# Kernel tuning notes

Measured on AMD Instinct MI355X. Metric: run time of the kernel, lower is better.

Reference implementation:

```python
import jax, jax.numpy as jnp
import numpy as np

B, S, D = 4, 1024, 1024
E, F, TOPK = 16, 512, 4


def setup_inputs() -> dict:
    key = jax.random.key(0)
    k1, k2, k3, k4, k5 = jax.random.split(key, 5)
    scale = 0.02
    return {
        "x": jax.random.normal(k1, (B, S, D), dtype=jnp.float32),
        "Wr": jax.random.normal(k2, (D, E), dtype=jnp.float32) * scale,   # router
        "Wg": jax.random.normal(k3, (E, D, F), dtype=jnp.float32) * scale,  # gate proj
        "Wu": jax.random.normal(k4, (E, D, F), dtype=jnp.float32) * scale,  # up proj
        "Wd": jax.random.normal(k5, (E, F, D), dtype=jnp.float32) * scale,  # down proj
    }


def reference(x, Wr, Wg, Wu, Wd):
    b, s, d = x.shape
    xf = x.reshape(-1, d)                      # [N, D], N = B*S
    n = xf.shape[0]
    e = Wr.shape[1]

    # --- router: softmax over experts, top-k, renormalized weights ---
    probs = jax.nn.softmax(xf @ Wr, axis=-1)   # [N, E]
    w, idx = jax.lax.top_k(probs, TOPK)        # [N, K], [N, K]
    w = w / jnp.sum(w, axis=-1, keepdims=True)

    # combine weights per (token, expert); zero for unselected experts.
    # Equivalent to the per-expert where/gather/scatter-add loop in torch.
    cw = jnp.zeros((n, e), dtype=xf.dtype).at[jnp.arange(n)[:, None], idx].add(w)

    # --- per-expert gated FFN (SwiGLU), combined with routing weights ---
    def body(acc, ws):
        wg, wu, wd, c = ws                     # [D,F], [D,F], [F,D], [N]
        h = jax.nn.silu(xf @ wg) * (xf @ wu)   # [N, F]
        return acc + c[:, None] * (h @ wd), None

    out, _ = jax.lax.scan(body, jnp.zeros_like(xf), (Wg, Wu, Wd, cw.T))
    return out.reshape(b, s, d)
```

## Files before the change

kernel.cpp:

```cpp
#include <hip/hip_runtime.h>

#define N_TOK 4096
#define DIM   1024
#define NE    16
#define NF    512
#define TOPK  4
#define CAP   4096
#define NPAIR (N_TOK * TOPK)
#define MAXTILES 144

typedef _Float16 v8h __attribute__((ext_vector_type(8)));
typedef float    v4f __attribute__((ext_vector_type(4)));

__global__ __launch_bounds__(64) void router_kernel(
    const float* __restrict__ x, const float* __restrict__ Wr,
    int* __restrict__ tokIdx, float* __restrict__ tokW)
{
    int t = blockIdx.x;
    int l = threadIdx.x;
    double z[NE];
#pragma unroll
    for (int e = 0; e < NE; e++) z[e] = 0.0;
    const float* xrow = x + (size_t)t * DIM;
#pragma unroll
    for (int i = 0; i < 16; i++) {
        int d = i * 64 + l;
        double xv = (double)xrow[d];
        const float4* wr = (const float4*)(Wr + d * NE);
        float4 w0 = wr[0], w1 = wr[1], w2 = wr[2], w3 = wr[3];
        z[0]  += xv * w0.x; z[1]  += xv * w0.y; z[2]  += xv * w0.z; z[3]  += xv * w0.w;
        z[4]  += xv * w1.x; z[5]  += xv * w1.y; z[6]  += xv * w1.z; z[7]  += xv * w1.w;
        z[8]  += xv * w2.x; z[9]  += xv * w2.y; z[10] += xv * w2.z; z[11] += xv * w2.w;
        z[12] += xv * w3.x; z[13] += xv * w3.y; z[14] += xv * w3.z; z[15] += xv * w3.w;
    }
#pragma unroll
    for (int e = 0; e < NE; e++) {
#pragma unroll
        for (int m = 1; m < 64; m <<= 1) z[e] += __shfl_xor(z[e], m, 64);
    }
    if (l == 0) {
        bool taken[NE];
#pragma unroll
        for (int e = 0; e < NE; e++) taken[e] = false;
        int idx[TOPK]; double sel[TOPK];
        for (int k = 0; k < TOPK; k++) {
            int bi = 0; double bv = -1.0e300;
            for (int e = 0; e < NE; e++)
                if (!taken[e] && z[e] > bv) { bv = z[e]; bi = e; }
            taken[bi] = true; idx[k] = bi; sel[k] = bv;
        }
        double m = sel[0];
        double ex[TOPK]; double s = 0.0;
        for (int k = 0; k < TOPK; k++) { ex[k] = exp(sel[k] - m); s += ex[k]; }
        for (int k = 0; k < TOPK; k++) {
            tokIdx[t * TOPK + k] = idx[k];
            tokW[t * TOPK + k]   = (float)(ex[k] / s);
        }
    }
}

__global__ __launch_bounds__(1024) void bin_kernel(
    const int* __restrict__ tokIdx,
    int* __restrict__ cnt, int* __restrict__ ptile,
    int* __restrict__ tileE, int* __restrict__ tileMt,
    int* __restrict__ bpair)
{
    int wv = threadIdx.x >> 6;
    int lane = threadIdx.x & 63;
    __shared__ int scnt[NE];

    int c = 0;
    for (int i0 = lane * 4; i0 < NPAIR; i0 += 256) {
        int4 v = *(const int4*)(tokIdx + i0);
        c += (v.x == wv) + (v.y == wv) + (v.z == wv) + (v.w == wv);
    }
#pragma unroll
    for (int m = 1; m < 64; m <<= 1) c += __shfl_xor(c, m, 64);
    if (lane == 0) scnt[wv] = c;
    __syncthreads();
    if (threadIdx.x == 0) {
        int rt = 0;
        for (int e = 0; e < NE; e++) {
            cnt[e] = scnt[e];
            ptile[e] = rt;
            int nt = (scnt[e] + 127) >> 7;
            for (int t = 0; t < nt; t++) { tileE[rt + t] = e; tileMt[rt + t] = t; }
            rt += nt;
        }
        for (; rt < MAXTILES; rt++) tileE[rt] = -1;
    }

    int pos = 0;
    for (int i0b = 0; i0b < NPAIR; i0b += 256) {
        int i0 = i0b + lane * 4;
        int4 v = *(const int4*)(tokIdx + i0);
        int ev[4] = {v.x, v.y, v.z, v.w};
#pragma unroll
        for (int j = 0; j < 4; j++) {
            bool m = (ev[j] == wv);
            unsigned long long bal = __ballot(m);
            if (m) {
                int r = __popcll(bal & ((1ULL << lane) - 1ULL));
                bpair[wv * CAP + pos + r] = i0 + j;
            }
            pos += __popcll(bal);
        }
    }
}

__global__ __launch_bounds__(256) void cast_x_kernel(
    const float* __restrict__ x, unsigned short* __restrict__ xb)
{
    size_t base = ((size_t)blockIdx.x * 256 + threadIdx.x) * 8;
    float4 a = *(const float4*)(x + base);
    float4 b = *(const float4*)(x + base + 4);
    union { unsigned short u[8]; uint4 v; } p;
    p.u[0] = __builtin_bit_cast(unsigned short, (_Float16)a.x);
    p.u[1] = __builtin_bit_cast(unsigned short, (_Float16)a.y);
    p.u[2] = __builtin_bit_cast(unsigned short, (_Float16)a.z);
    p.u[3] = __builtin_bit_cast(unsigned short, (_Float16)a.w);
    p.u[4] = __builtin_bit_cast(unsigned short, (_Float16)b.x);
    p.u[5] = __builtin_bit_cast(unsigned short, (_Float16)b.y);
    p.u[6] = __builtin_bit_cast(unsigned short, (_Float16)b.z);
    p.u[7] = __builtin_bit_cast(unsigned short, (_Float16)b.w);
    *(uint4*)(xb + base) = p.v;
}

__global__ __launch_bounds__(256) void tile_weight_kernel(
    const float* __restrict__ src, unsigned short* __restrict__ dst,
    int R, int C, int RIL)
{
    __shared__ float tile[64][65];
    int e = blockIdx.z;
    const float* s = src + (size_t)e * R * C;
    int c0 = blockIdx.x * 64, r0 = blockIdx.y * 64;
    int t = threadIdx.x;
    int tr = t >> 4, tc = (t & 15) * 4;
#pragma unroll
    for (int i = 0; i < 4; i++) {
        int row = i * 16 + tr;
        float4 v = *(const float4*)(s + (size_t)(r0 + row) * C + c0 + tc);
        tile[row][tc + 0] = v.x; tile[row][tc + 1] = v.y;
        tile[row][tc + 2] = v.z; tile[row][tc + 3] = v.w;
    }
    __syncthreads();
    int ktPerE = R >> 5;
    int cbPerE = C >> RIL;
    int imgSz  = (1 << RIL) * 32;
#pragma unroll
    for (int i = 0; i < 4; i++) {
        int nr = i * 16 + tr;
        int orow = c0 + nr;
        int k0 = r0 + tc;
        int cb = orow >> RIL;
        int r  = orow & ((1 << RIL) - 1);
        int kt = k0 >> 5;
        size_t off = ((size_t)(e * cbPerE + cb) * ktPerE + kt) * imgSz
                   + r * 32 + (k0 & 31);
        union { unsigned short u[4]; uint2 v; } p;
#pragma unroll
        for (int j = 0; j < 4; j++)
            p.u[j] = __builtin_bit_cast(unsigned short, (_Float16)tile[tc + j][nr]);
        *(uint2*)(dst + off) = p.v;
    }
}

__device__ __forceinline__ int ldsw(int row, int chunk) {
    return row * 32 + (chunk ^ ((row >> 1) & 3)) * 8;
}

__global__ __launch_bounds__(256) void ffn_gate_up_kernel(
    const unsigned short* __restrict__ xb,
    const unsigned short* __restrict__ Wg_t,
    const unsigned short* __restrict__ Wu_t,
    const int* __restrict__ cnt, const int* __restrict__ ptile,
    const int* __restrict__ tileE, const int* __restrict__ tileMt,
    const int* __restrict__ bpair,
    unsigned short* __restrict__ h_t)
{
    int fb = blockIdx.x, ti = blockIdx.y;
    int e = tileE[ti];
    if (e < 0) return;
    int mt = tileMt[ti];
    int count = cnt[e];

    __shared__ __align__(16) unsigned short sX[128 * 32];
    __shared__ __align__(16) unsigned short sG[64 * 32];
    __shared__ __align__(16) unsigned short sU[64 * 32];
    __shared__ int sTok[128];

    int tid = threadIdx.x, lane = tid & 63, w = tid >> 6;
    if (tid < 128) {
        int pos = mt * 128 + tid;
        sTok[tid] = bpair[e * CAP + min(pos, count - 1)] >> 2;
    }
    __syncthreads();

    int xr0 = tid >> 2, xc = tid & 3;
    int xr1 = xr0 + 64;
    const unsigned short* gx0 = xb + (size_t)sTok[xr0] * DIM + xc * 8;
    const unsigned short* gx1 = xb + (size_t)sTok[xr1] * DIM + xc * 8;
    const unsigned short* gsrc = Wg_t + ((size_t)(e * 8 + fb) * 32) * 2048 + tid * 8;
    const unsigned short* usrc = Wu_t + ((size_t)(e * 8 + fb) * 32) * 2048 + tid * 8;

    unsigned short* wx0 = &sX[ldsw(xr0, xc)];
    unsigned short* wx1 = &sX[ldsw(xr1, xc)];
    unsigned short* wg  = &sG[ldsw(xr0, xc)];
    unsigned short* wu  = &sU[ldsw(xr0, xc)];

    int row = lane & 15, q = lane >> 4;
    int rw = w & 1, cw = w >> 1;
    int aoff[4], goff[2];
#pragma unroll
    for (int mi = 0; mi < 4; mi++) aoff[mi] = ldsw(rw * 64 + mi * 16 + row, q);
#pragma unroll
    for (int ni = 0; ni < 2; ni++) goff[ni] = ldsw(cw * 32 + ni * 16 + row, q);

    v4f accG[4][2], accU[4][2];
    v4f zero = {0.f, 0.f, 0.f, 0.f};
#pragma unroll
    for (int mi = 0; mi < 4; mi++)
#pragma unroll
        for (int ni = 0; ni < 2; ni++) { accG[mi][ni] = zero; accU[mi][ni] = zero; }

    uint4 rx0 = *(const uint4*)(gx0);
    uint4 rx1 = *(const uint4*)(gx1);
    uint4 rg  = *(const uint4*)(gsrc);
    uint4 ru  = *(const uint4*)(usrc);

#pragma unroll 1
    for (int kt = 0; kt < 32; kt++) {
        __syncthreads();
        *(uint4*)wx0 = rx0;
        *(uint4*)wx1 = rx1;
        *(uint4*)wg  = rg;
        *(uint4*)wu  = ru;
        if (kt < 31) {
            rx0 = *(const uint4*)(gx0 + (kt + 1) * 32);
            rx1 = *(const uint4*)(gx1 + (kt + 1) * 32);
            rg  = *(const uint4*)(gsrc + (size_t)(kt + 1) * 2048);
            ru  = *(const uint4*)(usrc + (size_t)(kt + 1) * 2048);
        }
        __syncthreads();
        v8h a[4], bg[2], bu[2];
#pragma unroll
        for (int mi = 0; mi < 4; mi++) a[mi] = *(const v8h*)&sX[aoff[mi]];
#pragma unroll
        for (int ni = 0; ni < 2; ni++) {
            bg[ni] = *(const v8h*)&sG[goff[ni]];
            bu[ni] = *(const v8h*)&sU[goff[ni]];
        }
#pragma unroll
        for (int mi = 0; mi < 4; mi++)
#pragma unroll
            for (int ni = 0; ni < 2; ni++) {
                accG[mi][ni] = __builtin_amdgcn_mfma_f32_16x16x32_f16(a[mi], bg[ni], accG[mi][ni], 0, 0, 0);
                accU[mi][ni] = __builtin_amdgcn_mfma_f32_16x16x32_f16(a[mi], bu[ni], accU[mi][ni], 0, 0, 0);
            }
    }

    size_t himg = (size_t)(ptile[e] + mt) * 16;
#pragma unroll
    for (int mi = 0; mi < 4; mi++)
#pragma unroll
        for (int ni = 0; ni < 2; ni++) {
            int f = fb * 64 + cw * 32 + ni * 16 + row;
#pragma unroll
            for (int i = 0; i < 4; i++) {
                int rl = rw * 64 + mi * 16 + q * 4 + i;
                int pos = mt * 128 + rl;
                if (pos < count) {
                    float gv = accG[mi][ni][i];
                    float uv = accU[mi][ni][i];
                    float hv = gv * uv / (1.0f + __expf(-gv));
                    size_t off = (himg + (f >> 5)) * 4096 + rl * 32 + (f & 31);
                    h_t[off] = __builtin_bit_cast(unsigned short, (_Float16)hv);
                }
            }
        }
}

__global__ __launch_bounds__(256) void ffn_down_kernel(
    const unsigned short* __restrict__ h_t,
    const unsigned short* __restrict__ Wd_t,
    const int* __restrict__ cnt, const int* __restrict__ ptile,
    const int* __restrict__ tileE, const int* __restrict__ tileMt,
    const int* __restrict__ bpair,
    unsigned short* __restrict__ part)
{
    int ti = blockIdx.x, db = blockIdx.y;
    int e = tileE[ti];
    if (e < 0) return;
    int mt = tileMt[ti];
    int count = cnt[e];

    __shared__ __align__(16) unsigned short sH[128 * 32];
    __shared__ __align__(16) unsigned short sW[128 * 32];
    __shared__ int sPair[128];

    int tid = threadIdx.x, lane = tid & 63, w = tid >> 6;
    if (tid < 128) {
        int pos = mt * 128 + tid;
        sPair[tid] = bpair[e * CAP + min(pos, count - 1)];
    }
    __syncthreads();

    int r0 = tid >> 2, c = tid & 3;
    int r1 = r0 + 64;
    const unsigned short* hsrc = h_t + ((size_t)(ptile[e] + mt) * 16) * 4096 + tid * 8;
    const unsigned short* wsrc = Wd_t + ((size_t)(e * 8 + db) * 16) * 4096 + tid * 8;

    unsigned short* wh0 = &sH[ldsw(r0, c)];
    unsigned short* wh1 = &sH[ldsw(r1, c)];
    unsigned short* ww0 = &sW[ldsw(r0, c)];
    unsigned short* ww1 = &sW[ldsw(r1, c)];

    int row = lane & 15, q = lane >> 4;
    int rw = w & 1, cw = w >> 1;
    int aoff[4], boff[4];
#pragma unroll
    for (int mi = 0; mi < 4; mi++) aoff[mi] = ldsw(rw * 64 + mi * 16 + row, q);
#pragma unroll
    for (int ni = 0; ni < 4; ni++) boff[ni] = ldsw(cw * 64 + ni * 16 + row, q);

    v4f acc[4][4];
    v4f zero = {0.f, 0.f, 0.f, 0.f};
#pragma unroll
    for (int mi = 0; mi < 4; mi++)
#pragma unroll
        for (int ni = 0; ni < 4; ni++) acc[mi][ni] = zero;

    uint4 rh0 = *(const uint4*)(hsrc);
    uint4 rh1 = *(const uint4*)(hsrc + 2048);
    uint4 rw0 = *(const uint4*)(wsrc);
    uint4 rw1 = *(const uint4*)(wsrc + 2048);

#pragma unroll 1
    for (int kt = 0; kt < 16; kt++) {
        __syncthreads();
        *(uint4*)wh0 = rh0;
        *(uint4*)wh1 = rh1;
        *(uint4*)ww0 = rw0;
        *(uint4*)ww1 = rw1;
        if (kt < 15) {
            rh0 = *(const uint4*)(hsrc + (size_t)(kt + 1) * 4096);
            rh1 = *(const uint4*)(hsrc + (size_t)(kt + 1) * 4096 + 2048);
            rw0 = *(const uint4*)(wsrc + (size_t)(kt + 1) * 4096);
            rw1 = *(const uint4*)(wsrc + (size_t)(kt + 1) * 4096 + 2048);
        }
        __syncthreads();
        v8h a[4], b[4];
#pragma unroll
        for (int mi = 0; mi < 4; mi++) a[mi] = *(const v8h*)&sH[aoff[mi]];
#pragma unroll
        for (int ni = 0; ni < 4; ni++) b[ni] = *(const v8h*)&sW[boff[ni]];
#pragma unroll
        for (int mi = 0; mi < 4; mi++)
#pragma unroll
            for (int ni = 0; ni < 4; ni++)
                acc[mi][ni] = __builtin_amdgcn_mfma_f32_16x16x32_f16(a[mi], b[ni], acc[mi][ni], 0, 0, 0);
    }

#pragma unroll
    for (int mi = 0; mi < 4; mi++)
#pragma unroll
        for (int ni = 0; ni < 4; ni++) {
            int col = db * 128 + cw * 64 + ni * 16 + row;
#pragma unroll
            for (int i = 0; i < 4; i++) {
                int rl = rw * 64 + mi * 16 + q * 4 + i;
                int pos = mt * 128 + rl;
                if (pos < count) {
                    int p = sPair[rl];
                    part[(size_t)p * DIM + col] =
                        __builtin_bit_cast(unsigned short, (_Float16)acc[mi][ni][i]);
                }
            }
        }
}

__global__ __launch_bounds__(256) void combine_kernel(
    const unsigned short* __restrict__ part, const float* __restrict__ tokW,
    float* __restrict__ out)
{
    int gid = blockIdx.x * 256 + threadIdx.x;
    int t = gid >> 8;
    int c = (gid & 255) * 4;
    float4 r = {0.f, 0.f, 0.f, 0.f};
#pragma unroll
    for (int k = 0; k < TOPK; k++) {
        float wk = tokW[t * TOPK + k];
        union { uint2 u; _Float16 h[4]; } cv;
        cv.u = *(const uint2*)(part + ((size_t)(t * TOPK + k)) * DIM + c);
        r.x += wk * (float)cv.h[0];
        r.y += wk * (float)cv.h[1];
        r.z += wk * (float)cv.h[2];
        r.w += wk * (float)cv.h[3];
    }
    *(float4*)(out + (size_t)t * DIM + c) = r;
}

extern "C" void kernel_launch(void* const* d_in, const int* in_sizes, int n_in,
                              void* d_out, int out_size, void* d_ws, size_t ws_size,
                              hipStream_t stream)
{
    const float* x  = (const float*)d_in[0];
    const float* Wr = (const float*)d_in[1];
    const float* Wg = (const float*)d_in[2];
    const float* Wu = (const float*)d_in[3];
    const float* Wd = (const float*)d_in[4];
    float* out = (float*)d_out;
    char* ws = (char*)d_ws;

    size_t off = 0;
    int* tokIdx = (int*)(ws + off);   off += (size_t)NPAIR * 4;
    float* tokW = (float*)(ws + off); off += (size_t)NPAIR * 4;
    int* cnt    = (int*)(ws + off);   off += 256;
    int* ptile  = (int*)(ws + off);   off += 256;
    int* tileE  = (int*)(ws + off);   off += MAXTILES * 4;
    int* tileMt = (int*)(ws + off);   off += MAXTILES * 4;
    int* bpair  = (int*)(ws + off);   off += (size_t)NE * CAP * 4;
    unsigned short* xb   = (unsigned short*)(ws + off); off += (size_t)N_TOK * DIM * 2;
    unsigned short* Wg_t = (unsigned short*)(ws + off); off += (size_t)NE * DIM * NF * 2;
    unsigned short* Wu_t = (unsigned short*)(ws + off); off += (size_t)NE * DIM * NF * 2;
    unsigned short* Wd_t = (unsigned short*)(ws + off); off += (size_t)NE * DIM * NF * 2;
    unsigned short* h_t  = (unsigned short*)(ws + off); off += (size_t)MAXTILES * 16 * 4096 * 2;
    unsigned short* part = (unsigned short*)(ws + off); off += (size_t)NPAIR * DIM * 2;

    router_kernel<<<N_TOK, 64, 0, stream>>>(x, Wr, tokIdx, tokW);
    bin_kernel<<<1, 1024, 0, stream>>>(tokIdx, cnt, ptile, tileE, tileMt, bpair);
    cast_x_kernel<<<(N_TOK * DIM) / (256 * 8), 256, 0, stream>>>(x, xb);
    tile_weight_kernel<<<dim3(NF / 64, DIM / 64, NE), 256, 0, stream>>>(Wg, Wg_t, DIM, NF, 6);
    tile_weight_kernel<<<dim3(NF / 64, DIM / 64, NE), 256, 0, stream>>>(Wu, Wu_t, DIM, NF, 6);
    tile_weight_kernel<<<dim3(DIM / 64, NF / 64, NE), 256, 0, stream>>>(Wd, Wd_t, NF, DIM, 7);
    ffn_gate_up_kernel<<<dim3(8, MAXTILES), 256, 0, stream>>>(
        xb, Wg_t, Wu_t, cnt, ptile, tileE, tileMt, bpair, h_t);
    ffn_down_kernel<<<dim3(MAXTILES, 8), 256, 0, stream>>>(
        h_t, Wd_t, cnt, ptile, tileE, tileMt, bpair, part);
    combine_kernel<<<(N_TOK * DIM) / (256 * 4), 256, 0, stream>>>(part, tokW, out);
}
```

Measured before the change: 325.2 us.

## Widen GEMM K-tile to 64, fuse x cast into router, merge weight prep

The x fp16 cast moves into the router kernel, and the three weight-tiling launches become one combined prep kernel, which removes launches and a separate pass over x. Both FFN GEMM kernels now stage K=64 per shared-memory tile with a new 8-way XOR swizzle, halving the number of barrier-separated iterations. Each iteration does two MFMA sub-steps, and the global prefetch is issued between them. This doubles LDS usage, which may reduce occupancy, and it depends on the weight-tiling layout still matching the new load indexing.

After: 512.9 us. 57.7% more time.

```diff
diff --git a/kernel.cpp b/kernel.cpp
--- a/kernel.cpp
+++ b/kernel.cpp
@@ -14,7 +14,8 @@
 
 __global__ __launch_bounds__(64) void router_kernel(
     const float* __restrict__ x, const float* __restrict__ Wr,
-    int* __restrict__ tokIdx, float* __restrict__ tokW)
+    int* __restrict__ tokIdx, float* __restrict__ tokW,
+    unsigned short* __restrict__ xb)
 {
     int t = blockIdx.x;
     int l = threadIdx.x;
@@ -32,6 +33,23 @@
         z[4]  += xv * w1.x; z[5]  += xv * w1.y; z[6]  += xv * w1.z; z[7]  += xv * w1.w;
         z[8]  += xv * w2.x; z[9]  += xv * w2.y; z[10] += xv * w2.z; z[11] += xv * w2.w;
         z[12] += xv * w3.x; z[13] += xv * w3.y; z[14] += xv * w3.z; z[15] += xv * w3.w;
+    }
+    const float4* xv4 = (const float4*)xrow;
+#pragma unroll
+    for (int h2 = 0; h2 < 2; h2++) {
+        int base = h2 * 512 + l * 8;
+        float4 a = xv4[h2 * 128 + l * 2];
+        float4 b = xv4[h2 * 128 + l * 2 + 1];
+        union { unsigned short u[8]; uint4 v; } p;
+        p.u[0] = __builtin_bit_cast(unsigned short, (_Float16)a.x);
+        p.u[1] = __builtin_bit_cast(unsigned short, (_Float16)a.y);
+        p.u[2] = __builtin_bit_cast(unsigned short, (_Float16)a.z);
+        p.u[3] = __builtin_bit_cast(unsigned short, (_Float16)a.w);
+        p.u[4] = __builtin_bit_cast(unsigned short, (_Float16)b.x);
+        p.u[5] = __builtin_bit_cast(unsigned short, (_Float16)b.y);
+        p.u[6] = __builtin_bit_cast(unsigned short, (_Float16)b.z);
+        p.u[7] = __builtin_bit_cast(unsigned short, (_Float16)b.w);
+        *(uint4*)(xb + (size_t)t * DIM + base) = p.v;
     }
 #pragma unroll
     for (int e = 0; e < NE; e++) {
@@ -108,32 +126,26 @@
     }
 }
 
-__global__ __launch_bounds__(256) void cast_x_kernel(
-    const float* __restrict__ x, unsigned short* __restrict__ xb)
-{
-    size_t base = ((size_t)blockIdx.x * 256 + threadIdx.x) * 8;
-    float4 a = *(const float4*)(x + base);
-    float4 b = *(const float4*)(x + base + 4);
-    union { unsigned short u[8]; uint4 v; } p;
-    p.u[0] = __builtin_bit_cast(unsigned short, (_Float16)a.x);
-    p.u[1] = __builtin_bit_cast(unsigned short, (_Float16)a.y);
-    p.u[2] = __builtin_bit_cast(unsigned short, (_Float16)a.z);
-    p.u[3] = __builtin_bit_cast(unsigned short, (_Float16)a.w);
-    p.u[4] = __builtin_bit_cast(unsigned short, (_Float16)b.x);
-    p.u[5] = __builtin_bit_cast(unsigned short, (_Float16)b.y);
-    p.u[6] = __builtin_bit_cast(unsigned short, (_Float16)b.z);
-    p.u[7] = __builtin_bit_cast(unsigned short, (_Float16)b.w);
-    *(uint4*)(xb + base) = p.v;
-}
-
-__global__ __launch_bounds__(256) void tile_weight_kernel(
-    const float* __restrict__ src, unsigned short* __restrict__ dst,
-    int R, int C, int RIL)
-{
+__global__ __launch_bounds__(256) void prep_weight_kernel(
+    const float* __restrict__ Wg, const float* __restrict__ Wu,
+    const float* __restrict__ Wd,
+    unsigned short* __restrict__ Wg_t, unsigned short* __restrict__ Wu_t,
+    unsigned short* __restrict__ Wd_t)
+{
+    int z = blockIdx.y;
+    int which = z >> 4, e = z & 15;
+    const float* src; unsigned short* dst; int R, C, RIL;
+    if (which == 0)      { src = Wg; dst = Wg_t; R = DIM; C = NF;  RIL = 6; }
+    else if (which == 1) { src = Wu; dst = Wu_t; R = DIM; C = NF;  RIL = 6; }
+    else                 { src = Wd; dst = Wd_t; R = NF;  C = DIM; RIL = 7; }
+    int bx = blockIdx.x;
+    int cbl, rbl;
+    if (which < 2) { cbl = bx & 7;  rbl = bx >> 3; }
+    else           { cbl = bx & 15; rbl = bx >> 4; }
+    int c0 = cbl * 64, r0 = rbl * 64;
+
     __shared__ float tile[64][65];
-    int e = blockIdx.z;
     const float* s = src + (size_t)e * R * C;
-    int c0 = blockIdx.x * 64, r0 = blockIdx.y * 64;
     int t = threadIdx.x;
     int tr = t >> 4, tc = (t & 15) * 4;
 #pragma unroll
@@ -165,8 +177,8 @@
     }
 }
 
-__device__ __forceinline__ int ldsw(int row, int chunk) {
-    return row * 32 + (chunk ^ ((row >> 1) & 3)) * 8;
+__device__ __forceinline__ int ldsw64(int row, int chunk) {
+    return row * 64 + (chunk ^ (row & 7)) * 8;
 }
 
 __global__ __launch_bounds__(256) void ffn_gate_up_kernel(
@@ -184,9 +196,9 @@
     int mt = tileMt[ti];
     int count = cnt[e];
 
-    __shared__ __align__(16) unsigned short sX[128 * 32];
-    __shared__ __align__(16) unsigned short sG[64 * 32];
-    __shared__ __align__(16) unsigned short sU[64 * 32];
+    __shared__ __align__(16) unsigned short sX[128 * 64];
+    __shared__ __align__(16) unsigned short sG[64 * 64];
+    __shared__ __align__(16) unsigned short sU[64 * 64];
     __shared__ int sTok[128];
 
     int tid = threadIdx.x, lane = tid & 63, w = tid >> 6;
@@ -196,25 +208,36 @@
     }
     __syncthreads();
 
-    int xr0 = tid >> 2, xc = tid & 3;
-    int xr1 = xr0 + 64;
-    const unsigned short* gx0 = xb + (size_t)sTok[xr0] * DIM + xc * 8;
-    const unsigned short* gx1 = xb + (size_t)sTok[xr1] * DIM + xc * 8;
-    const unsigned short* gsrc = Wg_t + ((size_t)(e * 8 + fb) * 32) * 2048 + tid * 8;
-    const unsigned short* usrc = Wu_t + ((size_t)(e * 8 + fb) * 32) * 2048 + tid * 8;
-
-    unsigned short* wx0 = &sX[ldsw(xr0, xc)];
-    unsigned short* wx1 = &sX[ldsw(xr1, xc)];
-    unsigned short* wg  = &sG[ldsw(xr0, xc)];
-    unsigned short* wu  = &sU[ldsw(xr0, xc)];
+    int xr = tid >> 1, xcb = (tid & 1) * 4;
+    const unsigned short* xsrc = xb + (size_t)sTok[xr] * DIM + xcb * 8;
+    unsigned short* xdst[4];
+#pragma unroll
+    for (int j = 0; j < 4; j++) xdst[j] = &sX[ldsw64(xr, xcb + j)];
+
+    const unsigned short* gW = Wg_t + (size_t)(e * 8 + fb) * 65536 + (size_t)(2 * tid) * 8;
+    const unsigned short* gU = Wu_t + (size_t)(e * 8 + fb) * 65536 + (size_t)(2 * tid) * 8;
+    int wrr = (tid >> 1) & 63;
+    unsigned short* gdst[2]; unsigned short* udst[2];
+#pragma unroll
+    for (int j = 0; j < 2; j++) {
+        int g = 2 * tid + j;
+        int c = (g >> 8) * 4 + (g & 3);
+        gdst[j] = &sG[ldsw64(wrr, c)];
+        udst[j] = &sU[ldsw64(wrr, c)];
+    }
 
     int row = lane & 15, q = lane >> 4;
     int rw = w & 1, cw = w >> 1;
-    int aoff[4], goff[2];
-#pragma unroll
-    for (int mi = 0; mi < 4; mi++) aoff[mi] = ldsw(rw * 64 + mi * 16 + row, q);
-#pragma unroll
-    for (int ni = 0; ni < 2; ni++) goff[ni] = ldsw(cw * 32 + ni * 16 + row, q);
+    int aoff[2][4], goff[2][2];
+#pragma unroll
+    for (int kk = 0; kk < 2; kk++) {
+#pragma unroll
+        for (int mi = 0; mi < 4; mi++)
+            aoff[kk][mi] = ldsw64(rw * 64 + mi * 16 + row, kk * 4 + q);
+#pragma unroll
+        for (int ni = 0; ni < 2; ni++)
+            goff[kk][ni] = ldsw64(cw * 32 + ni * 16 + row, kk * 4 + q);
+    }
 
     v4f accG[4][2], accU[4][2];
     v4f zero = {0.f, 0.f, 0.f, 0.f};
@@ -223,32 +246,54 @@
 #pragma unroll
         for (int ni = 0; ni < 2; ni++) { accG[mi][ni] = zero; accU[mi][ni] = zero; }
 
-    uint4 rx0 = *(const uint4*)(gx0);
-    uint4 rx1 = *(const uint4*)(gx1);
-    uint4 rg  = *(const uint4*)(gsrc);
-    uint4 ru  = *(const uint4*)(usrc);
+    uint4 px[4], pg[2], pu[2];
+#pragma unroll
+    for (int j = 0; j < 4; j++) px[j] = *(const uint4*)(xsrc + j * 8);
+#pragma unroll
+    for (int j = 0; j < 2; j++) {
+        pg[j] = *(const uint4*)(gW + j * 8);
+        pu[j] = *(const uint4*)(gU + j * 8);
+    }
 
 #pragma unroll 1
-    for (int kt = 0; kt < 32; kt++) {
+    for (int s = 0; s < 16; s++) {
         __syncthreads();
-        *(uint4*)wx0 = rx0;
-        *(uint4*)wx1 = rx1;
-        *(uint4*)wg  = rg;
-        *(uint4*)wu  = ru;
-        if (kt < 31) {
-            rx0 = *(const uint4*)(gx0 + (kt + 1) * 32);
-            rx1 = *(const uint4*)(gx1 + (kt + 1) * 32);
-            rg  = *(const uint4*)(gsrc + (size_t)(kt + 1) * 2048);
-            ru  = *(const uint4*)(usrc + (size_t)(kt + 1) * 2048);
-        }
+#pragma unroll
+        for (int j = 0; j < 4; j++) *(uint4*)xdst[j] = px[j];
+#pragma unroll
+        for (int j = 0; j < 2; j++) { *(uint4*)gdst[j] = pg[j]; *(uint4*)udst[j] = pu[j]; }
         __syncthreads();
         v8h a[4], bg[2], bu[2];
 #pragma unroll
-        for (int mi = 0; mi < 4; mi++) a[mi] = *(const v8h*)&sX[aoff[mi]];
+        for (int mi = 0; mi < 4; mi++) a[mi] = *(const v8h*)&sX[aoff[0][mi]];
 #pragma unroll
         for (int ni = 0; ni < 2; ni++) {
-            bg[ni] = *(const v8h*)&sG[goff[ni]];
-            bu[ni] = *(const v8h*)&sU[goff[ni]];
+            bg[ni] = *(const v8h*)&sG[goff[0][ni]];
+            bu[ni] = *(const v8h*)&sU[goff[0][ni]];
+        }
+        if (s < 15) {
+#pragma unroll
+            for (int j = 0; j < 4; j++)
+                px[j] = *(const uint4*)(xsrc + (s + 1) * 64 + j * 8);
+#pragma unroll
+            for (int j = 0; j < 2; j++) {
+                pg[j] = *(const uint4*)(gW + (size_t)(s + 1) * 4096 + j * 8);
+                pu[j] = *(const uint4*)(gU + (size_t)(s + 1) * 4096 + j * 8);
+            }
+        }
+#pragma unroll
+        for (int mi = 0; mi < 4; mi++)
+#pragma unroll
+            for (int ni = 0; ni < 2; ni++) {
+                accG[mi][ni] = __builtin_amdgcn_mfma_f32_16x16x32_f16(a[mi], bg[ni], accG[mi][ni], 0, 0, 0);
+                accU[mi][ni] = __builtin_amdgcn_mfma_f32_16x16x32_f16(a[mi], bu[ni], accU[mi][ni], 0, 0, 0);
+            }
+#pragma unroll
+        for (int mi = 0; mi < 4; mi++) a[mi] = *(const v8h*)&sX[aoff[1][mi]];
+#pragma unroll
+        for (int ni = 0; ni < 2; ni++) {
+            bg[ni] = *(const v8h*)&sG[goff[1][ni]];
+            bu[ni] = *(const v8h*)&sU[goff[1][ni]];
         }
 #pragma unroll
         for (int mi = 0; mi < 4; mi++)
@@ -294,8 +339,8 @@
     int mt = tileMt[ti];
     int count = cnt[e];
 
-    __shared__ __align__(16) unsigned short sH[128 * 32];
-    __shared__ __align__(16) unsigned short sW[128 * 32];
+    __shared__ __align__(16) unsigned short sH[128 * 64];
+    __shared__ __align__(16) unsigned short sW[128 * 64];
     __shared__ int sPair[128];
 
     int tid = threadIdx.x, lane = tid & 63, w = tid >> 6;
@@ -305,23 +350,30 @@
     }
     __syncthreads();
 
-    int r0 = tid >> 2, c = tid & 3;
-    int r1 = r0 + 64;
-    const unsigned short* hsrc = h_t + ((size_t)(ptile[e] + mt) * 16) * 4096 + tid * 8;
-    const unsigned short* wsrc = Wd_t + ((size_t)(e * 8 + db) * 16) * 4096 + tid * 8;
-
-    unsigned short* wh0 = &sH[ldsw(r0, c)];
-    unsigned short* wh1 = &sH[ldsw(r1, c)];
-    unsigned short* ww0 = &sW[ldsw(r0, c)];
-    unsigned short* ww1 = &sW[ldsw(r1, c)];
+    const unsigned short* hsrc = h_t + (size_t)(ptile[e] + mt) * 65536 + (size_t)tid * 8;
+    const unsigned short* wsrc = Wd_t + (size_t)(e * 8 + db) * 65536 + (size_t)tid * 8;
+    unsigned short* hdst[4]; unsigned short* wdst[4];
+#pragma unroll
+    for (int j = 0; j < 4; j++) {
+        int g = j * 256 + tid;
+        int r = (g >> 2) & 127;
+        int c = (g >> 9) * 4 + (tid & 3);
+        hdst[j] = &sH[ldsw64(r, c)];
+        wdst[j] = &sW[ldsw64(r, c)];
+    }
 
     int row = lane & 15, q = lane >> 4;
     int rw = w & 1, cw = w >> 1;
-    int aoff[4], boff[4];
-#pragma unroll
-    for (int mi = 0; mi < 4; mi++) aoff[mi] = ldsw(rw * 64 + mi * 16 + row, q);
-#pragma unroll
-    for (int ni = 0; ni < 4; ni++) boff[ni] = ldsw(cw * 64 + ni * 16 + row, q);
+    int aoff[2][4], boff[2][4];
+#pragma unroll
+    for (int kk = 0; kk < 2; kk++) {
+#pragma unroll
+        for (int mi = 0; mi < 4; mi++)
+            aoff[kk][mi] = ldsw64(rw * 64 + mi * 16 + row, kk * 4 + q);
+#pragma unroll
+        for (int ni = 0; ni < 4; ni++)
+            boff[kk][ni] = ldsw64(cw * 64 + ni * 16 + row, kk * 4 + q);
+    }
 
     v4f acc[4][4];
     v4f zero = {0.f, 0.f, 0.f, 0.f};
@@ -330,30 +382,40 @@
 #pragma unroll
         for (int ni = 0; ni < 4; ni++) acc[mi][ni] = zero;
 
-    uint4 rh0 = *(const uint4*)(hsrc);
-    uint4 rh1 = *(const uint4*)(hsrc + 2048);
-    uint4 rw0 = *(const uint4*)(wsrc);
-    uint4 rw1 = *(const uint4*)(wsrc + 2048);
+    uint4 ph[4], pw[4];
+#pragma unroll
+    for (int j = 0; j < 4; j++) {
+        ph[j] = *(const uint4*)(hsrc + (size_t)j * 2048);
+        pw[j] = *(const uint4*)(wsrc + (size_t)j * 2048);
+    }
 
 #pragma unroll 1
-    for (int kt = 0; kt < 16; kt++) {
+    for (int s = 0; s < 8; s++) {
         __syncthreads();
-        *(uint4*)wh0 = rh0;
-        *(uint4*)wh1 = rh1;
-        *(uint4*)ww0 = rw0;
-        *(uint4*)ww1 = rw1;
-        if (kt < 15) {
-            rh0 = *(const uint4*)(hsrc + (size_t)(kt + 1) * 4096);
-            rh1 = *(const uint4*)(hsrc + (size_t)(kt + 1) * 4096 + 2048);
-            rw0 = *(const uint4*)(wsrc + (size_t)(kt + 1) * 4096);
-            rw1 = *(const uint4*)(wsrc + (size_t)(kt + 1) * 4096 + 2048);
-        }
+#pragma unroll
+        for (int j = 0; j < 4; j++) { *(uint4*)hdst[j] = ph[j]; *(uint4*)wdst[j] = pw[j]; }
         __syncthreads();
         v8h a[4], b[4];
 #pragma unroll
-        for (int mi = 0; mi < 4; mi++) a[mi] = *(const v8h*)&sH[aoff[mi]];
-#pragma unroll
-        for (int ni = 0; ni < 4; ni++) b[ni] = *(const v8h*)&sW[boff[ni]];
+        for (int mi = 0; mi < 4; mi++) a[mi] = *(const v8h*)&sH[aoff[0][mi]];
+#pragma unroll
+        for (int ni = 0; ni < 4; ni++) b[ni] = *(const v8h*)&sW[boff[0][ni]];
+        if (s < 7) {
+#pragma unroll
+            for (int j = 0; j < 4; j++) {
+                ph[j] = *(const uint4*)(hsrc + (size_t)(s + 1) * 8192 + (size_t)j * 2048);
+                pw[j] = *(const uint4*)(wsrc + (size_t)(s + 1) * 8192 + (size_t)j * 2048);
+            }
+        }
+#pragma unroll
+        for (int mi = 0; mi < 4; mi++)
+#pragma unroll
+            for (int ni = 0; ni < 4; ni++)
+                acc[mi][ni] = __builtin_amdgcn_mfma_f32_16x16x32_f16(a[mi], b[ni], acc[mi][ni], 0, 0, 0);
+#pragma unroll
+        for (int mi = 0; mi < 4; mi++) a[mi] = *(const v8h*)&sH[aoff[1][mi]];
+#pragma unroll
+        for (int ni = 0; ni < 4; ni++) b[ni] = *(const v8h*)&sW[boff[1][ni]];
 #pragma unroll
         for (int mi = 0; mi < 4; mi++)
 #pragma unroll
@@ -427,12 +489,9 @@
     unsigned short* h_t  = (unsigned short*)(ws + off); off += (size_t)MAXTILES * 16 * 4096 * 2;
     unsigned short* part = (unsigned short*)(ws + off); off += (size_t)NPAIR * DIM * 2;
 
-    router_kernel<<<N_TOK, 64, 0, stream>>>(x, Wr, tokIdx, tokW);
+    router_kernel<<<N_TOK, 64, 0, stream>>>(x, Wr, tokIdx, tokW, xb);
     bin_kernel<<<1, 1024, 0, stream>>>(tokIdx, cnt, ptile, tileE, tileMt, bpair);
-    cast_x_kernel<<<(N_TOK * DIM) / (256 * 8), 256, 0, stream>>>(x, xb);
-    tile_weight_kernel<<<dim3(NF / 64, DIM / 64, NE), 256, 0, stream>>>(Wg, Wg_t, DIM, NF, 6);
-    tile_weight_kernel<<<dim3(NF / 64, DIM / 64, NE), 256, 0, stream>>>(Wu, Wu_t, DIM, NF, 6);
-    tile_weight_kernel<<<dim3(DIM / 64, NF / 64, NE), 256, 0, stream>>>(Wd, Wd_t, NF, DIM, 7);
+    prep_weight_kernel<<<dim3(128, 48), 256, 0, stream>>>(Wg, Wu, Wd, Wg_t, Wu_t, Wd_t);
     ffn_gate_up_kernel<<<dim3(8, MAXTILES), 256, 0, stream>>>(
         xb, Wg_t, Wu_t, cnt, ptile, tileE, tileMt, bpair, h_t);
     ffn_down_kernel<<<dim3(MAXTILES, 8), 256, 0, stream>>>(
```

## Fuse x cast into router, parallelize binning per expert, merge weight prep launches

Applied to the files above, without the earlier changes.

The fp16 cast of x now runs inside the router kernel, which already reads each token row, so the separate cast kernel and its second read of x are gone. Binning moves from one 1024-thread block to one 256-thread block per expert, using a block-level ballot prefix scan. The tile table is dropped and each FFN block recomputes its expert and tile from the counts. The three weight-tiling launches become one grid. Fewer launches and a parallel binning step are traded for a short serial tile-lookup loop at the start of every FFN block.

New measurement: 288.7 us. 11.2% less time.

```diff
diff --git a/kernel.cpp b/kernel.cpp
--- a/kernel.cpp
+++ b/kernel.cpp
@@ -14,7 +14,8 @@
 
 __global__ __launch_bounds__(64) void router_kernel(
     const float* __restrict__ x, const float* __restrict__ Wr,
-    int* __restrict__ tokIdx, float* __restrict__ tokW)
+    int* __restrict__ tokIdx, float* __restrict__ tokW,
+    unsigned short* __restrict__ xb)
 {
     int t = blockIdx.x;
     int l = threadIdx.x;
@@ -33,6 +34,23 @@
         z[8]  += xv * w2.x; z[9]  += xv * w2.y; z[10] += xv * w2.z; z[11] += xv * w2.w;
         z[12] += xv * w3.x; z[13] += xv * w3.y; z[14] += xv * w3.z; z[15] += xv * w3.w;
     }
+    const float4* xv4 = (const float4*)xrow;
+#pragma unroll
+    for (int h2 = 0; h2 < 2; h2++) {
+        int base = h2 * 512 + l * 8;
+        float4 a = xv4[h2 * 128 + l * 2];
+        float4 b = xv4[h2 * 128 + l * 2 + 1];
+        union { unsigned short u[8]; uint4 v; } p;
+        p.u[0] = __builtin_bit_cast(unsigned short, (_Float16)a.x);
+        p.u[1] = __builtin_bit_cast(unsigned short, (_Float16)a.y);
+        p.u[2] = __builtin_bit_cast(unsigned short, (_Float16)a.z);
+        p.u[3] = __builtin_bit_cast(unsigned short, (_Float16)a.w);
+        p.u[4] = __builtin_bit_cast(unsigned short, (_Float16)b.x);
+        p.u[5] = __builtin_bit_cast(unsigned short, (_Float16)b.y);
+        p.u[6] = __builtin_bit_cast(unsigned short, (_Float16)b.z);
+        p.u[7] = __builtin_bit_cast(unsigned short, (_Float16)b.w);
+        *(uint4*)(xb + (size_t)t * DIM + base) = p.v;
+    }
 #pragma unroll
     for (int e = 0; e < NE; e++) {
 #pragma unroll
@@ -59,81 +77,63 @@
     }
 }
 
-__global__ __launch_bounds__(1024) void bin_kernel(
+__global__ __launch_bounds__(256) void bin_kernel(
     const int* __restrict__ tokIdx,
-    int* __restrict__ cnt, int* __restrict__ ptile,
-    int* __restrict__ tileE, int* __restrict__ tileMt,
-    int* __restrict__ bpair)
-{
-    int wv = threadIdx.x >> 6;
-    int lane = threadIdx.x & 63;
-    __shared__ int scnt[NE];
-
-    int c = 0;
-    for (int i0 = lane * 4; i0 < NPAIR; i0 += 256) {
+    int* __restrict__ cnt, int* __restrict__ bpair)
+{
+    int e = blockIdx.x;
+    int tid = threadIdx.x, lane = tid & 63, wv = tid >> 6;
+    __shared__ int wsum[4];
+    __shared__ int sbase;
+    if (tid == 0) sbase = 0;
+    __syncthreads();
+    unsigned long long lt = (1ULL << lane) - 1ULL;
+#pragma unroll 1
+    for (int c0 = 0; c0 < NPAIR; c0 += 1024) {
+        int i0 = c0 + tid * 4;
         int4 v = *(const int4*)(tokIdx + i0);
-        c += (v.x == wv) + (v.y == wv) + (v.z == wv) + (v.w == wv);
-    }
-#pragma unroll
-    for (int m = 1; m < 64; m <<= 1) c += __shfl_xor(c, m, 64);
-    if (lane == 0) scnt[wv] = c;
-    __syncthreads();
-    if (threadIdx.x == 0) {
-        int rt = 0;
-        for (int e = 0; e < NE; e++) {
-            cnt[e] = scnt[e];
-            ptile[e] = rt;
-            int nt = (scnt[e] + 127) >> 7;
-            for (int t = 0; t < nt; t++) { tileE[rt + t] = e; tileMt[rt + t] = t; }
-            rt += nt;
-        }
-        for (; rt < MAXTILES; rt++) tileE[rt] = -1;
-    }
-
-    int pos = 0;
-    for (int i0b = 0; i0b < NPAIR; i0b += 256) {
-        int i0 = i0b + lane * 4;
-        int4 v = *(const int4*)(tokIdx + i0);
-        int ev[4] = {v.x, v.y, v.z, v.w};
+        int m[4] = {v.x == e, v.y == e, v.z == e, v.w == e};
+        int r[4]; int wcnt = 0;
 #pragma unroll
         for (int j = 0; j < 4; j++) {
-            bool m = (ev[j] == wv);
-            unsigned long long bal = __ballot(m);
-            if (m) {
-                int r = __popcll(bal & ((1ULL << lane) - 1ULL));
-                bpair[wv * CAP + pos + r] = i0 + j;
-            }
-            pos += __popcll(bal);
-        }
-    }
-}
-
-__global__ __launch_bounds__(256) void cast_x_kernel(
-    const float* __restrict__ x, unsigned short* __restrict__ xb)
-{
-    size_t base = ((size_t)blockIdx.x * 256 + threadIdx.x) * 8;
-    float4 a = *(const float4*)(x + base);
-    float4 b = *(const float4*)(x + base + 4);
-    union { unsigned short u[8]; uint4 v; } p;
-    p.u[0] = __builtin_bit_cast(unsigned short, (_Float16)a.x);
-    p.u[1] = __builtin_bit_cast(unsigned short, (_Float16)a.y);
-    p.u[2] = __builtin_bit_cast(unsigned short, (_Float16)a.z);
-    p.u[3] = __builtin_bit_cast(unsigned short, (_Float16)a.w);
-    p.u[4] = __builtin_bit_cast(unsigned short, (_Float16)b.x);
-    p.u[5] = __builtin_bit_cast(unsigned short, (_Float16)b.y);
-    p.u[6] = __builtin_bit_cast(unsigned short, (_Float16)b.z);
-    p.u[7] = __builtin_bit_cast(unsigned short, (_Float16)b.w);
-    *(uint4*)(xb + base) = p.v;
-}
-
-__global__ __launch_bounds__(256) void tile_weight_kernel(
-    const float* __restrict__ src, unsigned short* __restrict__ dst,
-    int R, int C, int RIL)
-{
+            unsigned long long bal = __ballot(m[j] != 0);
+            r[j] = wcnt + __popcll(bal & lt);
+            wcnt += __popcll(bal);
+        }
+        if (lane == 0) wsum[wv] = wcnt;
+        __syncthreads();
+        int woff = sbase;
+        for (int k = 0; k < wv; k++) woff += wsum[k];
+#pragma unroll
+        for (int j = 0; j < 4; j++)
+            if (m[j]) bpair[e * CAP + woff + r[j]] = i0 + j;
+        __syncthreads();
+        if (tid == 0) sbase += wsum[0] + wsum[1] + wsum[2] + wsum[3];
+        __syncthreads();
+    }
+    if (tid == 0) cnt[e] = sbase;
+}
+
+__global__ __launch_bounds__(256) void prep_weight_kernel(
+    const float* __restrict__ Wg, const float* __restrict__ Wu,
+    const float* __restrict__ Wd,
+    unsigned short* __restrict__ Wg_t, unsigned short* __restrict__ Wu_t,
+    unsigned short* __restrict__ Wd_t)
+{
+    int z = blockIdx.y;
+    int which = z >> 4, e = z & 15;
+    const float* src; unsigned short* dst; int R, C, RIL;
+    if (which == 0)      { src = Wg; dst = Wg_t; R = DIM; C = NF;  RIL = 6; }
+    else if (which == 1) { src = Wu; dst = Wu_t; R = DIM; C = NF;  RIL = 6; }
+    else                 { src = Wd; dst = Wd_t; R = NF;  C = DIM; RIL = 7; }
+    int bx = blockIdx.x;
+    int cbl, rbl;
+    if (which < 2) { cbl = bx & 7;  rbl = bx >> 3; }
+    else           { cbl = bx & 15; rbl = bx >> 4; }
+    int c0 = cbl * 64, r0 = rbl * 64;
+
     __shared__ float tile[64][65];
-    int e = blockIdx.z;
     const float* s = src + (size_t)e * R * C;
-    int c0 = blockIdx.x * 64, r0 = blockIdx.y * 64;
     int t = threadIdx.x;
     int tr = t >> 4, tc = (t & 15) * 4;
 #pragma unroll
@@ -169,19 +169,29 @@
     return row * 32 + (chunk ^ ((row >> 1) & 3)) * 8;
 }
 
+__device__ __forceinline__ bool find_tile(const int* __restrict__ cnt,
+                                          int ti, int& e, int& mt, int& tbase) {
+    int rt = 0;
+#pragma unroll 1
+    for (int ee = 0; ee < NE; ee++) {
+        int nt = (cnt[ee] + 127) >> 7;
+        if (ti < rt + nt) { e = ee; mt = ti - rt; tbase = rt; return true; }
+        rt += nt;
+    }
+    return false;
+}
+
 __global__ __launch_bounds__(256) void ffn_gate_up_kernel(
     const unsigned short* __restrict__ xb,
     const unsigned short* __restrict__ Wg_t,
     const unsigned short* __restrict__ Wu_t,
-    const int* __restrict__ cnt, const int* __restrict__ ptile,
-    const int* __restrict__ tileE, const int* __restrict__ tileMt,
+    const int* __restrict__ cnt,
     const int* __restrict__ bpair,
     unsigned short* __restrict__ h_t)
 {
     int fb = blockIdx.x, ti = blockIdx.y;
-    int e = tileE[ti];
-    if (e < 0) return;
-    int mt = tileMt[ti];
+    int e, mt, tbase;
+    if (!find_tile(cnt, ti, e, mt, tbase)) return;
     int count = cnt[e];
 
     __shared__ __align__(16) unsigned short sX[128 * 32];
@@ -259,7 +269,7 @@
             }
     }
 
-    size_t himg = (size_t)(ptile[e] + mt) * 16;
+    size_t himg = (size_t)(tbase + mt) * 16;
 #pragma unroll
     for (int mi = 0; mi < 4; mi++)
 #pragma unroll
@@ -283,15 +293,13 @@
 __global__ __launch_bounds__(256) void ffn_down_kernel(
     const unsigned short* __restrict__ h_t,
     const unsigned short* __restrict__ Wd_t,
-    const int* __restrict__ cnt, const int* __restrict__ ptile,
-    const int* __restrict__ tileE, const int* __restrict__ tileMt,
+    const int* __restrict__ cnt,
     const int* __restrict__ bpair,
     unsigned short* __restrict__ part)
 {
     int ti = blockIdx.x, db = blockIdx.y;
-    int e = tileE[ti];
-    if (e < 0) return;
-    int mt = tileMt[ti];
+    int e, mt, tbase;
+    if (!find_tile(cnt, ti, e, mt, tbase)) return;
     int count = cnt[e];
 
     __shared__ __align__(16) unsigned short sH[128 * 32];
@@ -307,7 +315,7 @@
 
     int r0 = tid >> 2, c = tid & 3;
     int r1 = r0 + 64;
-    const unsigned short* hsrc = h_t + ((size_t)(ptile[e] + mt) * 16) * 4096 + tid * 8;
+    const unsigned short* hsrc = h_t + ((size_t)(tbase + mt) * 16) * 4096 + tid * 8;
     const unsigned short* wsrc = Wd_t + ((size_t)(e * 8 + db) * 16) * 4096 + tid * 8;
 
     unsigned short* wh0 = &sH[ldsw(r0, c)];
@@ -416,9 +424,6 @@
     int* tokIdx = (int*)(ws + off);   off += (size_t)NPAIR * 4;
     float* tokW = (float*)(ws + off); off += (size_t)NPAIR * 4;
     int* cnt    = (int*)(ws + off);   off += 256;
-    int* ptile  = (int*)(ws + off);   off += 256;
-    int* tileE  = (int*)(ws + off);   off += MAXTILES * 4;
-    int* tileMt = (int*)(ws + off);   off += MAXTILES * 4;
     int* bpair  = (int*)(ws + off);   off += (size_t)NE * CAP * 4;
     unsigned short* xb   = (unsigned short*)(ws + off); off += (size_t)N_TOK * DIM * 2;
     unsigned short* Wg_t = (unsigned short*)(ws + off); off += (size_t)NE * DIM * NF * 2;
@@ -427,15 +432,12 @@
     unsigned short* h_t  = (unsigned short*)(ws + off); off += (size_t)MAXTILES * 16 * 4096 * 2;
     unsigned short* part = (unsigned short*)(ws + off); off += (size_t)NPAIR * DIM * 2;
 
-    router_kernel<<<N_TOK, 64, 0, stream>>>(x, Wr, tokIdx, tokW);
-    bin_kernel<<<1, 1024, 0, stream>>>(tokIdx, cnt, ptile, tileE, tileMt, bpair);
-    cast_x_kernel<<<(N_TOK * DIM) / (256 * 8), 256, 0, stream>>>(x, xb);
-    tile_weight_kernel<<<dim3(NF / 64, DIM / 64, NE), 256, 0, stream>>>(Wg, Wg_t, DIM, NF, 6);
-    tile_weight_kernel<<<dim3(NF / 64, DIM / 64, NE), 256, 0, stream>>>(Wu, Wu_t, DIM, NF, 6);
-    tile_weight_kernel<<<dim3(DIM / 64, NF / 64, NE), 256, 0, stream>>>(Wd, Wd_t, NF, DIM, 7);
+    router_kernel<<<N_TOK, 64, 0, stream>>>(x, Wr, tokIdx, tokW, xb);
+    bin_kernel<<<NE, 256, 0, stream>>>(tokIdx, cnt, bpair);
+    prep_weight_kernel<<<dim3(128, 48), 256, 0, stream>>>(Wg, Wu, Wd, Wg_t, Wu_t, Wd_t);
     ffn_gate_up_kernel<<<dim3(8, MAXTILES), 256, 0, stream>>>(
-        xb, Wg_t, Wu_t, cnt, ptile, tileE, tileMt, bpair, h_t);
+        xb, Wg_t, Wu_t, cnt, bpair, h_t);
     ffn_down_kernel<<<dim3(MAXTILES, 8), 256, 0, stream>>>(
-        h_t, Wd_t, cnt, ptile, tileE, tileMt, bpair, part);
+        h_t, Wd_t, cnt, bpair, part);
     combine_kernel<<<(N_TOK * DIM) / (256 * 4), 256, 0, stream>>>(part, tokW, out);
 }
```
